# Kernel tuning notes

Measured on AMD Instinct MI355X. Metric: run time of the kernel, lower is better.

## Reference

```python
import jax, jax.numpy as jnp
import numpy as np

N = 50000   # nodes in both graphs
E = 800000  # edges per graph
IN = 128
OUT = 64
NEG_SLOPE = 0.2  # DGL GATConv default


def setup_inputs() -> dict:
    key = jax.random.key(0)
    ks = jax.random.split(key, 12)
    stdv = 1.0 / np.sqrt(OUT)
    return {
        'h': jax.random.normal(ks[0], (N, IN), dtype=jnp.float32),
        'src0': jax.random.randint(ks[1], (E,), 0, N, dtype=jnp.int32),
        'dst0': jax.random.randint(ks[2], (E,), 0, N, dtype=jnp.int32),
        'row2': jax.random.randint(ks[3], (E,), 0, N, dtype=jnp.int32),
        'col2': jax.random.randint(ks[4], (E,), 0, N, dtype=jnp.int32),
        'adj_val': jax.random.uniform(ks[5], (E,), dtype=jnp.float32),
        # GATConv params (1 head)
        'W_gat': jax.random.normal(ks[6], (IN, OUT), dtype=jnp.float32) * 0.1,
        'attn_l': jax.random.normal(ks[7], (OUT,), dtype=jnp.float32) * 0.1,
        'attn_r': jax.random.normal(ks[8], (OUT,), dtype=jnp.float32) * 0.1,
        'bias_gat': jnp.zeros((OUT,), dtype=jnp.float32),
        # GraphConvolution params
        'W_gc': jax.random.uniform(ks[9], (IN, OUT), minval=-stdv, maxval=stdv, dtype=jnp.float32),
        'bias_gc': jax.random.uniform(ks[10], (OUT,), minval=-stdv, maxval=stdv, dtype=jnp.float32),
    }


def reference(h, src0, dst0, row2, col2, adj_val, W_gat, attn_l, attn_r, bias_gat, W_gc, bias_gc):
    n = h.shape[0]
    # ---- branch 0: GATConv(1 head) + elu activation ----
    feat = h @ W_gat                        # [N, OUT]
    el = feat @ attn_l                      # [N]
    er = feat @ attn_r                      # [N]
    e = el[src0] + er[dst0]                 # [E]
    e = jnp.where(e > 0, e, NEG_SLOPE * e)  # leaky_relu
    # edge softmax over incoming edges of each dst (stable)
    m = jax.ops.segment_max(e, dst0, num_segments=n)
    ex = jnp.exp(e - m[dst0])
    s = jax.ops.segment_sum(ex, dst0, num_segments=n)
    alpha = ex / s[dst0]                    # [E]
    agg = jax.ops.segment_sum(alpha[:, None] * feat[src0], dst0, num_segments=n)
    z1 = jax.nn.elu(agg + bias_gat)         # [N, OUT]
    # ---- branch 1: GraphConvolution: elu(adj @ (h @ W) + b) ----
    support = h @ W_gc                      # [N, OUT]
    gc = jax.ops.segment_sum(adj_val[:, None] * support[col2], row2, num_segments=n)
    z2 = jax.nn.elu(gc + bias_gc)           # [N, OUT]
    # ---- semantic attention tail (forward is just split+concat) ----
    return jnp.concatenate((z1, z2), axis=1)  # [N, 2*OUT]
```

## Files before the change

### kernel.cpp

```cpp
#include <hip/hip_runtime.h>
#include <hip/hip_bf16.h>
#include <math.h>

#define IN_F 128
#define OUT_F 64
#define BKT_SH 7
#define BKT_MASK 127
#define CHUNK 4096
#define MAXTB 1600
#define IDX_BITS 25

typedef __attribute__((ext_vector_type(8))) short bf16x8;
typedef __attribute__((ext_vector_type(4))) float f32x4;

__device__ inline short f2bf(float x) {
    __hip_bfloat16 b = __float2bfloat16(x);
    return *reinterpret_cast<short*>(&b);
}
__device__ inline float bflo(unsigned u) { return __uint_as_float(u << 16); }
__device__ inline float bfhi(unsigned u) { return __uint_as_float(u & 0xffff0000u); }

__global__ __launch_bounds__(256) void k_fused(const float* __restrict__ h,
                                               const float* __restrict__ Wg,
                                               const float* __restrict__ Wc,
                                               const float* __restrict__ attn_l,
                                               const float* __restrict__ attn_r,
                                               __hip_bfloat16* __restrict__ feat,
                                               __hip_bfloat16* __restrict__ support,
                                               float* __restrict__ el,
                                               float* __restrict__ er, int n, int G1,
                                               const int* __restrict__ dst0,
                                               const int* __restrict__ row2,
                                               int* __restrict__ bcnt,
                                               int* __restrict__ chunkhist,
                                               int NB, int E_) {
    __shared__ short Wl[16][128][8];
    __shared__ int hist[MAXTB];

    if ((int)blockIdx.x >= G1) {
        int TB = 2 * NB;
        int t = threadIdx.x;
        int chunk = (int)blockIdx.x - G1;
        for (int i = t; i < TB; i += 256) hist[i] = 0;
        __syncthreads();
        int e0 = chunk * CHUNK;
        for (int i = t; i < CHUNK; i += 256) {
            int e = e0 + i;
            if (e < E_) {
                atomicAdd(&hist[dst0[e] >> BKT_SH], 1);
                atomicAdd(&hist[NB + (row2[e] >> BKT_SH)], 1);
            }
        }
        __syncthreads();
        int* hrow = chunkhist + (size_t)chunk * TB;
        for (int b = t; b < TB; b += 256) {
            int c = hist[b];
            hrow[b] = c;
            if (c) atomicAdd(&bcnt[b], c);
        }
        return;
    }

    for (int i = threadIdx.x; i < 128 * 32; i += 256) {
        int k = i >> 5;
        int c4 = (i & 31) << 2;
        float4 v4 = (c4 < 64) ? *(const float4*)(Wg + k * 64 + c4)
                              : *(const float4*)(Wc + k * 64 + (c4 - 64));
        short* dst = &Wl[k >> 3][c4][k & 7];
        dst[0]  = f2bf(v4.x);
        dst[8]  = f2bf(v4.y);
        dst[16] = f2bf(v4.z);
        dst[24] = f2bf(v4.w);
    }
    __syncthreads();

    int lane = threadIdx.x & 63;
    int wv = threadIdx.x >> 6;
    int li = lane & 15, lg = lane >> 4;
    int row0 = blockIdx.x * 64 + wv * 16;

    f32x4 acc[8];
#pragma unroll
    for (int ct = 0; ct < 8; ++ct) acc[ct] = (f32x4){0.f, 0.f, 0.f, 0.f};

    int ar = row0 + li;
    if (ar >= n) ar = n - 1;
    const float* hrow = h + (size_t)ar * IN_F + lg * 8;
#pragma unroll
    for (int q = 0; q < 4; ++q) {
        float4 a0 = *(const float4*)(hrow + q * 32);
        float4 a1 = *(const float4*)(hrow + q * 32 + 4);
        bf16x8 af;
        af[0] = f2bf(a0.x); af[1] = f2bf(a0.y); af[2] = f2bf(a0.z); af[3] = f2bf(a0.w);
        af[4] = f2bf(a1.x); af[5] = f2bf(a1.y); af[6] = f2bf(a1.z); af[7] = f2bf(a1.w);
        int kg = q * 4 + lg;
#pragma unroll
        for (int ct = 0; ct < 8; ++ct) {
            bf16x8 bfr = *(const bf16x8*)&Wl[kg][ct * 16 + li][0];
            acc[ct] = __builtin_amdgcn_mfma_f32_16x16x32_bf16(af, bfr, acc[ct], 0, 0, 0);
        }
    }

    float alv[4], arv[4];
#pragma unroll
    for (int ct = 0; ct < 4; ++ct) {
        alv[ct] = attn_l[ct * 16 + li];
        arv[ct] = attn_r[ct * 16 + li];
    }
#pragma unroll
    for (int r = 0; r < 4; ++r) {
        int row = row0 + lg * 4 + r;
        float pl = 0.f, pr = 0.f;
#pragma unroll
        for (int ct = 0; ct < 4; ++ct) {
            pl += acc[ct][r] * alv[ct];
            pr += acc[ct][r] * arv[ct];
        }
#pragma unroll
        for (int m = 8; m; m >>= 1) {
            pl += __shfl_xor(pl, m);
            pr += __shfl_xor(pr, m);
        }
        if (li == 0 && row < n) { el[row] = pl; er[row] = pr; }
    }

#pragma unroll
    for (int r = 0; r < 4; ++r) {
        int row = row0 + lg * 4 + r;
        if (row >= n) continue;
#pragma unroll
        for (int ct = 0; ct < 4; ++ct)
            feat[(size_t)row * OUT_F + ct * 16 + li] = __float2bfloat16(acc[ct][r]);
#pragma unroll
        for (int ct = 4; ct < 8; ++ct)
            support[(size_t)row * OUT_F + (ct - 4) * 16 + li] = __float2bfloat16(acc[ct][r]);
    }
}

__global__ __launch_bounds__(256) void k_bscan(const int* __restrict__ bcnt,
                                               int* __restrict__ boffs, int nb2,
                                               int grand, int* __restrict__ offs, int tot) {
    __shared__ int sh[256];
    int t = threadIdx.x;
    int base = t * 8;
    int v[8];
    int sum = 0;
#pragma unroll
    for (int i = 0; i < 8; ++i) {
        int idx = base + i;
        v[i] = (idx < nb2) ? bcnt[idx] : 0;
        sum += v[i];
    }
    sh[t] = sum;
    __syncthreads();
    for (int off = 1; off < 256; off <<= 1) {
        int x = (t >= off) ? sh[t - off] : 0;
        __syncthreads();
        sh[t] += x;
        __syncthreads();
    }
    int run = sh[t] - sum;
#pragma unroll
    for (int i = 0; i < 8; ++i) {
        int idx = base + i;
        if (idx < nb2) boffs[idx] = run;
        run += v[i];
    }
    if (t == 0) { boffs[nb2] = grand; offs[tot] = grand; }
}

__global__ __launch_bounds__(256) void k_part(const int* __restrict__ src0,
                                              const int* __restrict__ dst0,
                                              const int* __restrict__ row2,
                                              const int* __restrict__ boffs,
                                              const int* __restrict__ chunkhist,
                                              int* __restrict__ gfill,
                                              unsigned* __restrict__ tmp, int NB, int E_) {
    __shared__ int hist[MAXTB];
    __shared__ int rbase[MAXTB];
    int TB = 2 * NB;
    int t = threadIdx.x;
    const int* hrow = chunkhist + (size_t)blockIdx.x * TB;
    for (int b = t; b < TB; b += 256) {
        int c = hrow[b];
        int bb = 0;
        if (c) bb = boffs[b] + atomicAdd(&gfill[b], c);
        rbase[b] = bb;
        hist[b] = 0;
    }
    __syncthreads();
    int e0 = blockIdx.x * CHUNK;
    for (int i = t; i < CHUNK; i += 256) {
        int e = e0 + i;
        if (e < E_) {
            int d = dst0[e];
            int b = d >> BKT_SH;
            int p = atomicAdd(&hist[b], 1);
            tmp[(size_t)rbase[b] + p] =
                ((unsigned)(d & BKT_MASK) << IDX_BITS) | (unsigned)src0[e];
            int r = row2[e];
            int b2 = NB + (r >> BKT_SH);
            int p2 = atomicAdd(&hist[b2], 1);
            tmp[(size_t)rbase[b2] + p2] =
                ((unsigned)(r & BKT_MASK) << IDX_BITS) | (unsigned)e;
        }
    }
}

__global__ __launch_bounds__(256) void k_bbuild(const unsigned* __restrict__ tmp,
                                                const int* __restrict__ boffs,
                                                const float* __restrict__ el,
                                                const float* __restrict__ er,
                                                const int* __restrict__ col2,
                                                const float* __restrict__ adj_val,
                                                int* __restrict__ offs,
                                                int2* __restrict__ ew, int NB, int n) {
    __shared__ int hcnt[128], hoff[128], hfill[128], sh[128];
    __shared__ float er_lds[128];
    int b = blockIdx.x;
    int t = threadIdx.x;
    int base = boffs[b];
    int cnt = boffs[b + 1] - base;
    bool isGat = b < NB;
    int nodeBase = (isGat ? b : b - NB) << BKT_SH;
    int offsBase = (isGat ? 0 : n) + nodeBase;

    if (t < 128) {
        hcnt[t] = 0;
        hfill[t] = 0;
        if (isGat && nodeBase + t < n) er_lds[t] = er[nodeBase + t];
    }
    __syncthreads();
    for (int i = t; i < cnt; i += 256)
        atomicAdd(&hcnt[tmp[(size_t)base + i] >> IDX_BITS], 1);
    __syncthreads();
    if (t < 128) sh[t] = hcnt[t];
    __syncthreads();
    for (int off = 1; off < 128; off <<= 1) {
        int x = (t < 128 && t >= off) ? sh[t - off] : 0;
        __syncthreads();
        if (t < 128) sh[t] += x;
        __syncthreads();
    }
    if (t < 128) {
        hoff[t] = sh[t] - hcnt[t];
        if (nodeBase + t < n) offs[offsBase + t] = base + hoff[t];
    }
    __syncthreads();
    for (int i = t; i < cnt; i += 256) {
        unsigned v = tmp[(size_t)base + i];
        unsigned loc = v >> IDX_BITS;
        int idx = (int)(v & ((1u << IDX_BITS) - 1u));
        int2 payload;
        if (isGat) {
            float e = el[idx] + er_lds[loc];
            e = e > 0.f ? e : 0.2f * e;
            payload = make_int2(idx, __float_as_int(__expf(e)));
        } else {
            payload = make_int2(col2[idx], __float_as_int(adj_val[idx]));
        }
        int p = atomicAdd(&hfill[loc], 1);
        ew[(size_t)base + hoff[loc] + p] = payload;
    }
}

__global__ __launch_bounds__(256) void k_agg(const int2* __restrict__ ew,
                                             const int* __restrict__ offs,
                                             const __hip_bfloat16* __restrict__ feat,
                                             const __hip_bfloat16* __restrict__ support,
                                             const float* __restrict__ bias_gat,
                                             const float* __restrict__ bias_gc,
                                             float* __restrict__ out, int n) {
    int wave = (int)(((long long)blockIdx.x * blockDim.x + threadIdx.x) >> 6);
    int lane = threadIdx.x & 63;
    int nh = (n + 1) >> 1;
    if (wave >= 2 * nh) return;
    int half = lane >> 5;
    int ll = lane & 31;
    int es2 = ll >> 4;
    int fg = ll & 15;
    int sbase = half << 5;

    bool isGat = wave < nh;
    int node = (isGat ? wave : wave - nh) * 2 + half;
    bool nodeValid = node < n;
    int wid = (isGat ? 0 : n) + (nodeValid ? node : 0);
    int start = offs[wid];
    int deg = nodeValid ? offs[wid + 1] - start : 0;

    const uint2* fbase = (const uint2*)(isGat ? feat : support);
    float acc[4] = {0.f, 0.f, 0.f, 0.f};
    float sw = 0.f;

    for (int c0 = 0; c0 < deg; c0 += 32) {
        int cnt = min(32, deg - c0);
        bool valid = ll < cnt;
        int2 e = valid ? ew[(size_t)start + c0 + ll] : make_int2(0, 0);
        float w = __int_as_float(e.y);
        float ts = w;
        ts += __shfl_xor(ts, 1);  ts += __shfl_xor(ts, 2);
        ts += __shfl_xor(ts, 4);  ts += __shfl_xor(ts, 8);
        ts += __shfl_xor(ts, 16);
        sw += ts;
#pragma unroll 4
        for (int k = 0; k < cnt; k += 2) {
            int src = sbase + k + es2;
            float wk = __shfl(w, src);
            int ik = __shfl(e.x, src);
            uint2 pv = fbase[(size_t)ik * 16 + fg];
            acc[0] += wk * bflo(pv.x); acc[1] += wk * bfhi(pv.x);
            acc[2] += wk * bflo(pv.y); acc[3] += wk * bfhi(pv.y);
        }
    }
#pragma unroll
    for (int j = 0; j < 4; ++j) acc[j] += __shfl_xor(acc[j], 16);
    if (es2 == 0 && nodeValid) {
        float inv = isGat ? (deg > 0 ? __builtin_amdgcn_rcpf(sw) : 0.f) : 1.f;
        const float* bias = isGat ? bias_gat : bias_gc;
        int outoff = isGat ? 0 : OUT_F;
        float4 bb = *(const float4*)(bias + fg * 4);
        float z0 = acc[0] * inv + bb.x;
        float z1 = acc[1] * inv + bb.y;
        float z2 = acc[2] * inv + bb.z;
        float z3 = acc[3] * inv + bb.w;
        z0 = z0 > 0.f ? z0 : __expf(z0) - 1.f;
        z1 = z1 > 0.f ? z1 : __expf(z1) - 1.f;
        z2 = z2 > 0.f ? z2 : __expf(z2) - 1.f;
        z3 = z3 > 0.f ? z3 : __expf(z3) - 1.f;
        *(float4*)(out + (size_t)node * 128 + outoff + fg * 4) = make_float4(z0, z1, z2, z3);
    }
}

extern "C" void kernel_launch(void* const* d_in, const int* in_sizes, int n_in,
                              void* d_out, int out_size, void* d_ws, size_t ws_size,
                              hipStream_t stream) {
    const float* h        = (const float*)d_in[0];
    const int*   src0     = (const int*)d_in[1];
    const int*   dst0     = (const int*)d_in[2];
    const int*   row2     = (const int*)d_in[3];
    const int*   col2     = (const int*)d_in[4];
    const float* adj_val  = (const float*)d_in[5];
    const float* Wg       = (const float*)d_in[6];
    const float* attn_l   = (const float*)d_in[7];
    const float* attn_r   = (const float*)d_in[8];
    const float* bias_gat = (const float*)d_in[9];
    const float* Wc       = (const float*)d_in[10];
    const float* bias_gc  = (const float*)d_in[11];

    int n  = in_sizes[0] / IN_F;
    int E_ = in_sizes[1];
    float* out = (float*)d_out;

    int NB = (n + BKT_MASK) >> BKT_SH;
    int TB = 2 * NB;
    if (TB > MAXTB) return;
    if (n >= (1 << IDX_BITS) || E_ >= (1 << IDX_BITS)) return;

    int nchunk = (E_ + CHUNK - 1) / CHUNK;

    char* p = (char*)d_ws;
    auto alloc = [&](size_t bytes, size_t align) -> void* {
        size_t a = ((size_t)p + align - 1) & ~(align - 1);
        p = (char*)(a + bytes);
        return (void*)a;
    };
    unsigned* tmp = (unsigned*)alloc(2 * (size_t)E_ * sizeof(unsigned), 256);
    int2*  ew    = (int2*) alloc(2 * (size_t)E_ * sizeof(int2), 256);
    int*   offs  = (int*)  alloc((2 * (size_t)n + 1) * sizeof(int), 16);
    float* el    = (float*)alloc((size_t)n * sizeof(float), 16);
    float* er    = (float*)alloc((size_t)n * sizeof(float), 16);
    int*   bcnt  = (int*)  alloc(2 * (size_t)TB * sizeof(int), 16);
    int*   gfill = bcnt + TB;
    int*   boffs = (int*)  alloc(((size_t)TB + 1) * sizeof(int), 16);
    int*   chunkhist = (int*)alloc((size_t)nchunk * TB * sizeof(int), 16);
    __hip_bfloat16* feat    = (__hip_bfloat16*)alloc((size_t)n * OUT_F * sizeof(__hip_bfloat16), 256);
    __hip_bfloat16* support = (__hip_bfloat16*)alloc((size_t)n * OUT_F * sizeof(__hip_bfloat16), 256);
    size_t need = (size_t)(p - (char*)d_ws);
    if (ws_size < need) return;

    int G1 = (n + 63) / 64;

    hipMemsetAsync(bcnt, 0, 2 * (size_t)TB * sizeof(int), stream);
    k_fused<<<G1 + nchunk, 256, 0, stream>>>(h, Wg, Wc, attn_l, attn_r,
                                             feat, support, el, er, n, G1,
                                             dst0, row2, bcnt, chunkhist, NB, E_);
    k_bscan<<<1, 256, 0, stream>>>(bcnt, boffs, TB, 2 * E_, offs, 2 * n);
    k_part<<<nchunk, 256, 0, stream>>>(src0, dst0, row2, boffs, chunkhist,
                                       gfill, tmp, NB, E_);
    k_bbuild<<<TB, 256, 0, stream>>>(tmp, boffs, el, er, col2, adj_val,
                                     offs, ew, NB, n);
    int nh = (n + 1) >> 1;
    long long aggthreads = 2LL * nh * 64;
    k_agg<<<(int)((aggthreads + 255) / 256), 256, 0, stream>>>(
        ew, offs, feat, support, bias_gat, bias_gc, out, n);
}
```

Baseline: 134.7 us.

## Precompute edge weights in partition pass and pad global bucket counters

Moves the GAT edge-weight computation and the col2/adj_val gather from the bucket-build kernel into the partition kernel, which writes int2 payloads so the bucket build becomes a pure local scatter. It also shrinks CHUNK so there are more partition blocks, pads the global bucket counters to separate cache lines to reduce atomic contention, and aliases the chunk histogram with the final edge buffer to save workspace. The cost is a wider temporary buffer (8 bytes per entry instead of 4) and more per-chunk histogram rows and global atomics. The new path runs only when the workspace is large enough.

```diff
diff --git a/kernel.cpp b/kernel.cpp
--- a/kernel.cpp
+++ b/kernel.cpp
@@ -6,9 +6,11 @@
 #define OUT_F 64
 #define BKT_SH 7
 #define BKT_MASK 127
-#define CHUNK 4096
+#define CHUNK 1024
 #define MAXTB 1600
 #define IDX_BITS 25
+#define IDX_MASK ((1u << IDX_BITS) - 1u)
+#define PAD 16
 
 typedef __attribute__((ext_vector_type(8))) short bf16x8;
 typedef __attribute__((ext_vector_type(4))) float f32x4;
@@ -56,7 +58,7 @@
         for (int b = t; b < TB; b += 256) {
             int c = hist[b];
             hrow[b] = c;
-            if (c) atomicAdd(&bcnt[b], c);
+            if (c) atomicAdd(&bcnt[b * PAD], c);
         }
         return;
     }
@@ -148,7 +150,7 @@
 #pragma unroll
     for (int i = 0; i < 8; ++i) {
         int idx = base + i;
-        v[i] = (idx < nb2) ? bcnt[idx] : 0;
+        v[i] = (idx < nb2) ? bcnt[idx * PAD] : 0;
         sum += v[i];
     }
     sh[t] = sum;
@@ -169,13 +171,20 @@
     if (t == 0) { boffs[nb2] = grand; offs[tot] = grand; }
 }
 
+template <bool WPREC>
 __global__ __launch_bounds__(256) void k_part(const int* __restrict__ src0,
                                               const int* __restrict__ dst0,
                                               const int* __restrict__ row2,
+                                              const int* __restrict__ col2,
+                                              const float* __restrict__ adj_val,
+                                              const float* __restrict__ el,
+                                              const float* __restrict__ er,
                                               const int* __restrict__ boffs,
                                               const int* __restrict__ chunkhist,
                                               int* __restrict__ gfill,
-                                              unsigned* __restrict__ tmp, int NB, int E_) {
+                                              unsigned* __restrict__ tmp1,
+                                              int2* __restrict__ tmp2,
+                                              int NB, int E_) {
     __shared__ int hist[MAXTB];
     __shared__ int rbase[MAXTB];
     int TB = 2 * NB;
@@ -184,7 +193,7 @@
     for (int b = t; b < TB; b += 256) {
         int c = hrow[b];
         int bb = 0;
-        if (c) bb = boffs[b] + atomicAdd(&gfill[b], c);
+        if (c) bb = boffs[b] + atomicAdd(&gfill[b * PAD], c);
         rbase[b] = bb;
         hist[b] = 0;
     }
@@ -193,21 +202,36 @@
     for (int i = t; i < CHUNK; i += 256) {
         int e = e0 + i;
         if (e < E_) {
+            int s = src0[e];
             int d = dst0[e];
             int b = d >> BKT_SH;
             int p = atomicAdd(&hist[b], 1);
-            tmp[(size_t)rbase[b] + p] =
-                ((unsigned)(d & BKT_MASK) << IDX_BITS) | (unsigned)src0[e];
             int r = row2[e];
             int b2 = NB + (r >> BKT_SH);
             int p2 = atomicAdd(&hist[b2], 1);
-            tmp[(size_t)rbase[b2] + p2] =
-                ((unsigned)(r & BKT_MASK) << IDX_BITS) | (unsigned)e;
-        }
-    }
-}
-
-__global__ __launch_bounds__(256) void k_bbuild(const unsigned* __restrict__ tmp,
+            if (WPREC) {
+                float w = el[s] + er[d];
+                w = w > 0.f ? w : 0.2f * w;
+                w = __expf(w);
+                tmp2[(size_t)rbase[b] + p] =
+                    make_int2((int)(((unsigned)(d & BKT_MASK) << IDX_BITS) | (unsigned)s),
+                              __float_as_int(w));
+                tmp2[(size_t)rbase[b2] + p2] =
+                    make_int2((int)(((unsigned)(r & BKT_MASK) << IDX_BITS) | (unsigned)col2[e]),
+                              __float_as_int(adj_val[e]));
+            } else {
+                tmp1[(size_t)rbase[b] + p] =
+                    ((unsigned)(d & BKT_MASK) << IDX_BITS) | (unsigned)s;
+                tmp1[(size_t)rbase[b2] + p2] =
+                    ((unsigned)(r & BKT_MASK) << IDX_BITS) | (unsigned)e;
+            }
+        }
+    }
+}
+
+template <bool WPREC>
+__global__ __launch_bounds__(256) void k_bbuild(const unsigned* __restrict__ tmp1,
+                                                const int2* __restrict__ tmp2,
                                                 const int* __restrict__ boffs,
                                                 const float* __restrict__ el,
                                                 const float* __restrict__ er,
@@ -228,11 +252,14 @@
     if (t < 128) {
         hcnt[t] = 0;
         hfill[t] = 0;
-        if (isGat && nodeBase + t < n) er_lds[t] = er[nodeBase + t];
-    }
-    __syncthreads();
-    for (int i = t; i < cnt; i += 256)
-        atomicAdd(&hcnt[tmp[(size_t)base + i] >> IDX_BITS], 1);
+        if (!WPREC && isGat && nodeBase + t < n) er_lds[t] = er[nodeBase + t];
+    }
+    __syncthreads();
+    for (int i = t; i < cnt; i += 256) {
+        unsigned x = WPREC ? (unsigned)tmp2[(size_t)base + i].x
+                           : tmp1[(size_t)base + i];
+        atomicAdd(&hcnt[x >> IDX_BITS], 1);
+    }
     __syncthreads();
     if (t < 128) sh[t] = hcnt[t];
     __syncthreads();
@@ -248,19 +275,26 @@
     }
     __syncthreads();
     for (int i = t; i < cnt; i += 256) {
-        unsigned v = tmp[(size_t)base + i];
-        unsigned loc = v >> IDX_BITS;
-        int idx = (int)(v & ((1u << IDX_BITS) - 1u));
-        int2 payload;
-        if (isGat) {
-            float e = el[idx] + er_lds[loc];
-            e = e > 0.f ? e : 0.2f * e;
-            payload = make_int2(idx, __float_as_int(__expf(e)));
+        if (WPREC) {
+            int2 v = tmp2[(size_t)base + i];
+            unsigned loc = ((unsigned)v.x) >> IDX_BITS;
+            int p = atomicAdd(&hfill[loc], 1);
+            ew[(size_t)base + hoff[loc] + p] = make_int2((int)((unsigned)v.x & IDX_MASK), v.y);
         } else {
-            payload = make_int2(col2[idx], __float_as_int(adj_val[idx]));
-        }
-        int p = atomicAdd(&hfill[loc], 1);
-        ew[(size_t)base + hoff[loc] + p] = payload;
+            unsigned v = tmp1[(size_t)base + i];
+            unsigned loc = v >> IDX_BITS;
+            int idx = (int)(v & IDX_MASK);
+            int2 payload;
+            if (isGat) {
+                float e = el[idx] + er_lds[loc];
+                e = e > 0.f ? e : 0.2f * e;
+                payload = make_int2(idx, __float_as_int(__expf(e)));
+            } else {
+                payload = make_int2(col2[idx], __float_as_int(adj_val[idx]));
+            }
+            int p = atomicAdd(&hfill[loc], 1);
+            ew[(size_t)base + hoff[loc] + p] = payload;
+        }
     }
 }
 
@@ -364,31 +398,52 @@
         p = (char*)(a + bytes);
         return (void*)a;
     };
-    unsigned* tmp = (unsigned*)alloc(2 * (size_t)E_ * sizeof(unsigned), 256);
-    int2*  ew    = (int2*) alloc(2 * (size_t)E_ * sizeof(int2), 256);
+    size_t Rbytes = 2 * (size_t)E_ * sizeof(int2);
+    if ((size_t)nchunk * TB * sizeof(int) > Rbytes) return;
+    char* R = (char*)alloc(Rbytes, 256);
+    int*  chunkhist = (int*)R;
+    int2* ew        = (int2*)R;
     int*   offs  = (int*)  alloc((2 * (size_t)n + 1) * sizeof(int), 16);
     float* el    = (float*)alloc((size_t)n * sizeof(float), 16);
     float* er    = (float*)alloc((size_t)n * sizeof(float), 16);
-    int*   bcnt  = (int*)  alloc(2 * (size_t)TB * sizeof(int), 16);
-    int*   gfill = bcnt + TB;
+    int*   bcnt  = (int*)  alloc(2 * (size_t)TB * PAD * sizeof(int), 64);
+    int*   gfill = bcnt + TB * PAD;
     int*   boffs = (int*)  alloc(((size_t)TB + 1) * sizeof(int), 16);
-    int*   chunkhist = (int*)alloc((size_t)nchunk * TB * sizeof(int), 16);
     __hip_bfloat16* feat    = (__hip_bfloat16*)alloc((size_t)n * OUT_F * sizeof(__hip_bfloat16), 256);
     __hip_bfloat16* support = (__hip_bfloat16*)alloc((size_t)n * OUT_F * sizeof(__hip_bfloat16), 256);
-    size_t need = (size_t)(p - (char*)d_ws);
-    if (ws_size < need) return;
+    size_t base_need = (size_t)(p - (char*)d_ws);
+
+    size_t need_w = base_need + 2 * (size_t)E_ * sizeof(int2) + 256;
+    bool wprec = (ws_size >= need_w);
+    unsigned* tmp1 = nullptr;
+    int2*     tmp2 = nullptr;
+    if (wprec) {
+        tmp2 = (int2*)alloc(2 * (size_t)E_ * sizeof(int2), 256);
+    } else {
+        tmp1 = (unsigned*)alloc(2 * (size_t)E_ * sizeof(unsigned), 256);
+        if (ws_size < (size_t)(p - (char*)d_ws)) return;
+    }
 
     int G1 = (n + 63) / 64;
 
-    hipMemsetAsync(bcnt, 0, 2 * (size_t)TB * sizeof(int), stream);
+    hipMemsetAsync(bcnt, 0, 2 * (size_t)TB * PAD * sizeof(int), stream);
     k_fused<<<G1 + nchunk, 256, 0, stream>>>(h, Wg, Wc, attn_l, attn_r,
                                              feat, support, el, er, n, G1,
                                              dst0, row2, bcnt, chunkhist, NB, E_);
     k_bscan<<<1, 256, 0, stream>>>(bcnt, boffs, TB, 2 * E_, offs, 2 * n);
-    k_part<<<nchunk, 256, 0, stream>>>(src0, dst0, row2, boffs, chunkhist,
-                                       gfill, tmp, NB, E_);
-    k_bbuild<<<TB, 256, 0, stream>>>(tmp, boffs, el, er, col2, adj_val,
-                                     offs, ew, NB, n);
+    if (wprec) {
+        k_part<true><<<nchunk, 256, 0, stream>>>(src0, dst0, row2, col2, adj_val,
+                                                 el, er, boffs, chunkhist,
+                                                 gfill, tmp1, tmp2, NB, E_);
+        k_bbuild<true><<<TB, 256, 0, stream>>>(tmp1, tmp2, boffs, el, er,
+                                               col2, adj_val, offs, ew, NB, n);
+    } else {
+        k_part<false><<<nchunk, 256, 0, stream>>>(src0, dst0, row2, col2, adj_val,
+                                                  el, er, boffs, chunkhist,
+                                                  gfill, tmp1, tmp2, NB, E_);
+        k_bbuild<false><<<TB, 256, 0, stream>>>(tmp1, tmp2, boffs, el, er,
+                                                col2, adj_val, offs, ew, NB, n);
+    }
     int nh = (n + 1) >> 1;
     long long aggthreads = 2LL * nh * 64;
     k_agg<<<(int)((aggthreads + 255) / 256), 256, 0, stream>>>(
```

Measured after the change: 174.6 us. 29.6% more time.

## Compute edge weights during partition, widen buckets, pad counters, alias workspace

Applied to the files above, without the earlier changes.

Edge weights (exp of leaky-relu attention logits, and the gathered col2/adj_val) are now computed in the partition pass. Edges are streamed there in original order, so the random el/er/col2/adj_val gathers become mostly coalesced reads, and the bucket-build kernel only re-sorts 8-byte payloads. Buckets grow from 128 to 256 nodes, which halves the bucket count and the scan size. Global bucket counters are padded to separate cache lines to reduce atomic contention. The chunk histogram now shares memory with the edge-weight output buffer. In exchange the temporary buffer doubles to 8 bytes per edge, adding write and read traffic, and node/edge index capacity drops to 24 bits.

```diff
diff --git a/kernel.cpp b/kernel.cpp
--- a/kernel.cpp
+++ b/kernel.cpp
@@ -4,11 +4,13 @@
 
 #define IN_F 128
 #define OUT_F 64
-#define BKT_SH 7
-#define BKT_MASK 127
+#define BKT_SH 8
+#define BKT_MASK 255
 #define CHUNK 4096
-#define MAXTB 1600
-#define IDX_BITS 25
+#define MAXTB 800
+#define IDX_BITS 24
+#define IDX_MASK ((1u << IDX_BITS) - 1u)
+#define PAD 16
 
 typedef __attribute__((ext_vector_type(8))) short bf16x8;
 typedef __attribute__((ext_vector_type(4))) float f32x4;
@@ -56,7 +58,7 @@
         for (int b = t; b < TB; b += 256) {
             int c = hist[b];
             hrow[b] = c;
-            if (c) atomicAdd(&bcnt[b], c);
+            if (c) atomicAdd(&bcnt[b * PAD], c);
         }
         return;
     }
@@ -142,13 +144,13 @@
                                                int grand, int* __restrict__ offs, int tot) {
     __shared__ int sh[256];
     int t = threadIdx.x;
-    int base = t * 8;
-    int v[8];
+    int base = t * 4;
+    int v[4];
     int sum = 0;
 #pragma unroll
-    for (int i = 0; i < 8; ++i) {
+    for (int i = 0; i < 4; ++i) {
         int idx = base + i;
-        v[i] = (idx < nb2) ? bcnt[idx] : 0;
+        v[i] = (idx < nb2) ? bcnt[idx * PAD] : 0;
         sum += v[i];
     }
     sh[t] = sum;
@@ -161,7 +163,7 @@
     }
     int run = sh[t] - sum;
 #pragma unroll
-    for (int i = 0; i < 8; ++i) {
+    for (int i = 0; i < 4; ++i) {
         int idx = base + i;
         if (idx < nb2) boffs[idx] = run;
         run += v[i];
@@ -172,10 +174,14 @@
 __global__ __launch_bounds__(256) void k_part(const int* __restrict__ src0,
                                               const int* __restrict__ dst0,
                                               const int* __restrict__ row2,
+                                              const int* __restrict__ col2,
+                                              const float* __restrict__ adj_val,
+                                              const float* __restrict__ el,
+                                              const float* __restrict__ er,
                                               const int* __restrict__ boffs,
                                               const int* __restrict__ chunkhist,
                                               int* __restrict__ gfill,
-                                              unsigned* __restrict__ tmp, int NB, int E_) {
+                                              int2* __restrict__ tmp, int NB, int E_) {
     __shared__ int hist[MAXTB];
     __shared__ int rbase[MAXTB];
     int TB = 2 * NB;
@@ -184,7 +190,7 @@
     for (int b = t; b < TB; b += 256) {
         int c = hrow[b];
         int bb = 0;
-        if (c) bb = boffs[b] + atomicAdd(&gfill[b], c);
+        if (c) bb = boffs[b] + atomicAdd(&gfill[b * PAD], c);
         rbase[b] = bb;
         hist[b] = 0;
     }
@@ -193,30 +199,31 @@
     for (int i = t; i < CHUNK; i += 256) {
         int e = e0 + i;
         if (e < E_) {
+            int s = src0[e];
             int d = dst0[e];
             int b = d >> BKT_SH;
             int p = atomicAdd(&hist[b], 1);
+            float w = el[s] + er[d];
+            w = w > 0.f ? w : 0.2f * w;
+            w = __expf(w);
             tmp[(size_t)rbase[b] + p] =
-                ((unsigned)(d & BKT_MASK) << IDX_BITS) | (unsigned)src0[e];
+                make_int2((int)(((unsigned)(d & BKT_MASK) << IDX_BITS) | (unsigned)s),
+                          __float_as_int(w));
             int r = row2[e];
             int b2 = NB + (r >> BKT_SH);
             int p2 = atomicAdd(&hist[b2], 1);
             tmp[(size_t)rbase[b2] + p2] =
-                ((unsigned)(r & BKT_MASK) << IDX_BITS) | (unsigned)e;
-        }
-    }
-}
-
-__global__ __launch_bounds__(256) void k_bbuild(const unsigned* __restrict__ tmp,
+                make_int2((int)(((unsigned)(r & BKT_MASK) << IDX_BITS) | (unsigned)col2[e]),
+                          __float_as_int(adj_val[e]));
+        }
+    }
+}
+
+__global__ __launch_bounds__(256) void k_bbuild(const int2* __restrict__ tmp,
                                                 const int* __restrict__ boffs,
-                                                const float* __restrict__ el,
-                                                const float* __restrict__ er,
-                                                const int* __restrict__ col2,
-                                                const float* __restrict__ adj_val,
                                                 int* __restrict__ offs,
                                                 int2* __restrict__ ew, int NB, int n) {
-    __shared__ int hcnt[128], hoff[128], hfill[128], sh[128];
-    __shared__ float er_lds[128];
+    __shared__ int hcnt[256], hoff[256], hfill[256], sh[256];
     int b = blockIdx.x;
     int t = threadIdx.x;
     int base = boffs[b];
@@ -225,42 +232,29 @@
     int nodeBase = (isGat ? b : b - NB) << BKT_SH;
     int offsBase = (isGat ? 0 : n) + nodeBase;
 
-    if (t < 128) {
-        hcnt[t] = 0;
-        hfill[t] = 0;
-        if (isGat && nodeBase + t < n) er_lds[t] = er[nodeBase + t];
-    }
+    hcnt[t] = 0;
+    hfill[t] = 0;
     __syncthreads();
     for (int i = t; i < cnt; i += 256)
-        atomicAdd(&hcnt[tmp[(size_t)base + i] >> IDX_BITS], 1);
-    __syncthreads();
-    if (t < 128) sh[t] = hcnt[t];
-    __syncthreads();
-    for (int off = 1; off < 128; off <<= 1) {
-        int x = (t < 128 && t >= off) ? sh[t - off] : 0;
-        __syncthreads();
-        if (t < 128) sh[t] += x;
-        __syncthreads();
-    }
-    if (t < 128) {
-        hoff[t] = sh[t] - hcnt[t];
-        if (nodeBase + t < n) offs[offsBase + t] = base + hoff[t];
-    }
+        atomicAdd(&hcnt[((unsigned)tmp[(size_t)base + i].x) >> IDX_BITS], 1);
+    __syncthreads();
+    sh[t] = hcnt[t];
+    __syncthreads();
+    for (int off = 1; off < 256; off <<= 1) {
+        int x = (t >= off) ? sh[t - off] : 0;
+        __syncthreads();
+        sh[t] += x;
+        __syncthreads();
+    }
+    hoff[t] = sh[t] - hcnt[t];
+    if (nodeBase + t < n) offs[offsBase + t] = base + hoff[t];
     __syncthreads();
     for (int i = t; i < cnt; i += 256) {
-        unsigned v = tmp[(size_t)base + i];
-        unsigned loc = v >> IDX_BITS;
-        int idx = (int)(v & ((1u << IDX_BITS) - 1u));
-        int2 payload;
-        if (isGat) {
-            float e = el[idx] + er_lds[loc];
-            e = e > 0.f ? e : 0.2f * e;
-            payload = make_int2(idx, __float_as_int(__expf(e)));
-        } else {
-            payload = make_int2(col2[idx], __float_as_int(adj_val[idx]));
-        }
+        int2 v = tmp[(size_t)base + i];
+        unsigned loc = ((unsigned)v.x) >> IDX_BITS;
         int p = atomicAdd(&hfill[loc], 1);
-        ew[(size_t)base + hoff[loc] + p] = payload;
+        ew[(size_t)base + hoff[loc] + p] =
+            make_int2((int)((unsigned)v.x & IDX_MASK), v.y);
     }
 }
 
@@ -364,15 +358,18 @@
         p = (char*)(a + bytes);
         return (void*)a;
     };
-    unsigned* tmp = (unsigned*)alloc(2 * (size_t)E_ * sizeof(unsigned), 256);
-    int2*  ew    = (int2*) alloc(2 * (size_t)E_ * sizeof(int2), 256);
+    size_t Rbytes = 2 * (size_t)E_ * sizeof(int2);
+    if ((size_t)nchunk * TB * sizeof(int) > Rbytes) return;
+    char* R = (char*)alloc(Rbytes, 256);
+    int*  chunkhist = (int*)R;
+    int2* ew        = (int2*)R;
+    int2*  tmp   = (int2*) alloc(2 * (size_t)E_ * sizeof(int2), 256);
     int*   offs  = (int*)  alloc((2 * (size_t)n + 1) * sizeof(int), 16);
     float* el    = (float*)alloc((size_t)n * sizeof(float), 16);
     float* er    = (float*)alloc((size_t)n * sizeof(float), 16);
-    int*   bcnt  = (int*)  alloc(2 * (size_t)TB * sizeof(int), 16);
-    int*   gfill = bcnt + TB;
+    int*   bcnt  = (int*)  alloc(2 * (size_t)TB * PAD * sizeof(int), 64);
+    int*   gfill = bcnt + TB * PAD;
     int*   boffs = (int*)  alloc(((size_t)TB + 1) * sizeof(int), 16);
-    int*   chunkhist = (int*)alloc((size_t)nchunk * TB * sizeof(int), 16);
     __hip_bfloat16* feat    = (__hip_bfloat16*)alloc((size_t)n * OUT_F * sizeof(__hip_bfloat16), 256);
     __hip_bfloat16* support = (__hip_bfloat16*)alloc((size_t)n * OUT_F * sizeof(__hip_bfloat16), 256);
     size_t need = (size_t)(p - (char*)d_ws);
@@ -380,15 +377,14 @@
 
     int G1 = (n + 63) / 64;
 
-    hipMemsetAsync(bcnt, 0, 2 * (size_t)TB * sizeof(int), stream);
+    hipMemsetAsync(bcnt, 0, 2 * (size_t)TB * PAD * sizeof(int), stream);
     k_fused<<<G1 + nchunk, 256, 0, stream>>>(h, Wg, Wc, attn_l, attn_r,
                                              feat, support, el, er, n, G1,
                                              dst0, row2, bcnt, chunkhist, NB, E_);
     k_bscan<<<1, 256, 0, stream>>>(bcnt, boffs, TB, 2 * E_, offs, 2 * n);
-    k_part<<<nchunk, 256, 0, stream>>>(src0, dst0, row2, boffs, chunkhist,
-                                       gfill, tmp, NB, E_);
-    k_bbuild<<<TB, 256, 0, stream>>>(tmp, boffs, el, er, col2, adj_val,
-                                     offs, ew, NB, n);
+    k_part<<<nchunk, 256, 0, stream>>>(src0, dst0, row2, col2, adj_val,
+                                       el, er, boffs, chunkhist, gfill, tmp, NB, E_);
+    k_bbuild<<<TB, 256, 0, stream>>>(tmp, boffs, offs, ew, NB, n);
     int nh = (n + 1) >> 1;
     long long aggthreads = 2LL * nh * 64;
     k_agg<<<(int)((aggthreads + 255) / 256), 256, 0, stream>>>(
```

New measurement: 121.4 us. -9.9%, faster.
